# Optimization experiments

Measured on AMD Instinct MI355X. Metric: run time of the kernel, lower is better.

Reference implementation:

```python
import jax, jax.numpy as jnp
import numpy as np

B = 16384          # batch
IN = 256           # input_dim
HID = [1024, 1024, 512]
K = 8              # num_mixtures
D = 16             # latent_dim
NT = D * (D + 1) // 2  # 136 packed tril components per mixture

_rows, _cols = np.tril_indices(D)          # row-major lower-tri order, same as nested loops
_rows = jnp.asarray(_rows); _cols = jnp.asarray(_cols)
_diag_mask = _rows == _cols                # [NT] bool


def setup_inputs() -> dict:
    key = jax.random.key(0)
    ks = jax.random.split(key, 12)

    def lin(k, fi, fo):
        kw, kb = jax.random.split(k)
        s = 1.0 / np.sqrt(fi)
        W = (jax.random.uniform(kw, (fi, fo), minval=-s, maxval=s)).astype(jnp.float32)
        b = (jax.random.uniform(kb, (fo,), minval=-s, maxval=s)).astype(jnp.float32)
        return W, b

    W0, b0 = lin(ks[0], IN, HID[0])
    W1, b1 = lin(ks[1], HID[0], HID[1])
    W2, b2 = lin(ks[2], HID[1], HID[2])
    Wpi, bpi = lin(ks[3], HID[2], K)
    Wmu, bmu = lin(ks[4], HID[2], K * D)
    Wt, bt = lin(ks[5], HID[2], K * NT)
    x = jax.random.normal(ks[6], (B, IN), dtype=jnp.float32)
    return dict(x=x, W0=W0, b0=b0, W1=W1, b1=b1, W2=W2, b2=b2,
                Wpi=Wpi, bpi=bpi, Wmu=Wmu, bmu=bmu, Wt=Wt, bt=bt)


def reference(x, W0, b0, W1, b1, W2, b2, Wpi, bpi, Wmu, bmu, Wt, bt):
    # MLP trunk: Linear + ReLU chain
    h = jax.nn.relu(x @ W0 + b0)
    h = jax.nn.relu(h @ W1 + b1)
    h = jax.nn.relu(h @ W2 + b2)
    # Heads
    pi_k = jax.nn.softmax(h @ Wpi + bpi, axis=1)                 # [B, K]
    mu_k = (h @ Wmu + bmu).reshape(-1, K, D)                     # [B, K, D]
    tc = (h @ Wt + bt).reshape(-1, K, NT)                        # [B, K, NT]
    # Fused cholesky-tril assembly: exp on diagonal entries, copy off-diagonal,
    # scattered into lower triangle in row-major (i, j<=i) order.
    vals = jnp.where(_diag_mask, jnp.exp(tc), tc)                # [B, K, NT]
    tril = jnp.zeros((tc.shape[0], K, D, D), dtype=tc.dtype)
    tril = tril.at[:, :, _rows, _cols].set(vals)                 # [B, K, D, D]
    return pi_k, mu_k, tril
```

## Files before the change

### kernel.cpp

```cpp
#include <hip/hip_runtime.h>
#include <hip/hip_bf16.h>
#include <cstdint>
#include <cstddef>

typedef __attribute__((ext_vector_type(8))) _Float16 half8;
typedef __attribute__((ext_vector_type(4))) float f32x4;
typedef __attribute__((ext_vector_type(8))) unsigned short ushort8v;
typedef __attribute__((ext_vector_type(4))) unsigned short ushort4v;

__device__ __forceinline__ unsigned short f2h_bits(float x) {
  _Float16 h = (_Float16)x;
  union { _Float16 h; unsigned short u; } cv; cv.h = h; return cv.u;
}

__device__ __forceinline__ void barrier_raw() {
  asm volatile("" ::: "memory");
  __builtin_amdgcn_s_barrier();
  asm volatile("" ::: "memory");
}
template<int N> __device__ __forceinline__ void vmw() {
  static_assert(N == 0 || N == 3 || N == 4, "unsupported vmcnt");
  if constexpr (N == 0) asm volatile("s_waitcnt vmcnt(0)" ::: "memory");
  if constexpr (N == 3) asm volatile("s_waitcnt vmcnt(3)" ::: "memory");
  if constexpr (N == 4) asm volatile("s_waitcnt vmcnt(4)" ::: "memory");
}
__device__ __forceinline__ void lgkm0() {
  asm volatile("s_waitcnt lgkmcnt(0)" ::: "memory");
}


__global__ __launch_bounds__(256) void k_transpose_f16(const float* __restrict__ W,
                                                       unsigned short* __restrict__ Wt,
                                                       int Kd, int N) {
  int tid = blockIdx.x * 256 + threadIdx.x;
  int total = (Kd >> 3) * N;
  if (tid >= total) return;
  int kc = tid / N;
  int n  = tid - kc * N;
  int k0 = kc << 3;
  ushort8v o;
#pragma unroll
  for (int j = 0; j < 8; ++j) o[j] = f2h_bits(W[(size_t)(k0 + j) * N + n]);
  *(ushort8v*)(&Wt[(size_t)n * Kd + k0]) = o;
}

__global__ __launch_bounds__(256) void k_build_head(
    const float* __restrict__ Wmu, const float* __restrict__ Wt,
    const float* __restrict__ Wpi,
    const float* __restrict__ bmu, const float* __restrict__ bt,
    const float* __restrict__ bpi,
    unsigned short* __restrict__ whd, float* __restrict__ bhd)
{
  int tid = blockIdx.x * 256 + threadIdx.x;
  if (tid >= 2304 * 64) return;
  int r  = tid >> 6;
  int d0 = (tid & 63) << 3;

  const float* src = nullptr; int stride = 0;
  if (r < 128) { src = Wmu + r; stride = 128; }
  else if (r < 2176) {
    int rU = r - 128, k = rU >> 8, i = (rU >> 4) & 15, j = rU & 15;
    if (j <= i) { src = Wt + k * 136 + ((i * (i + 1)) >> 1) + j; stride = 1088; }
  } else if (r < 2184) { src = Wpi + (r - 2176); stride = 8; }

  ushort8v o;
#pragma unroll
  for (int jj = 0; jj < 8; ++jj)
    o[jj] = src ? f2h_bits(src[(size_t)(d0 + jj) * stride]) : (unsigned short)0;
  *(ushort8v*)(&whd[(size_t)r * 512 + d0]) = o;

  if (d0 == 0) {
    float b = 0.f;
    if (r < 128) b = bmu[r];
    else if (r < 2176) {
      int rU = r - 128, k = rU >> 8, i = (rU >> 4) & 15, j = rU & 15;
      if (j <= i) b = bt[k * 136 + ((i * (i + 1)) >> 1) + j];
    } else if (r < 2184) b = bpi[r - 2176];
    bhd[r] = b;
  }
}


__device__ __forceinline__ void epi_relu_h(const f32x4& a, const float* bias, int col0,
                                           unsigned short* Hout, size_t row, int N) {
  float4 b4 = *(const float4*)&bias[col0];
  ushort4v o;
  float v0 = a[0] + b4.x; o[0] = f2h_bits(v0 > 0.f ? v0 : 0.f);
  float v1 = a[1] + b4.y; o[1] = f2h_bits(v1 > 0.f ? v1 : 0.f);
  float v2 = a[2] + b4.z; o[2] = f2h_bits(v2 > 0.f ? v2 : 0.f);
  float v3 = a[3] + b4.w; o[3] = f2h_bits(v3 > 0.f ? v3 : 0.f);
  *(ushort4v*)&Hout[row * N + col0] = o;
}

__device__ __forceinline__ void epi_head(const f32x4& a, const float* bias, int col0,
                                         size_t row, float* out_pi, float* out_mu,
                                         float* out_tril) {
  if (col0 >= 2184) return;
  float4 b4 = *(const float4*)&bias[col0];
  float v[4] = { a[0] + b4.x, a[1] + b4.y, a[2] + b4.z, a[3] + b4.w };
  if (col0 < 128) {
    *(float4*)&out_mu[row * 128 + col0] = make_float4(v[0], v[1], v[2], v[3]);
  } else if (col0 < 2176) {
    const int cc0 = col0 - 128;
    const int i   = (cc0 >> 4) & 15;
    const int j0  = cc0 & 15;
#pragma unroll
    for (int r = 0; r < 4; ++r) if (j0 + r == i) v[r] = expf(v[r]);
    *(float4*)&out_tril[row * 2048 + cc0] = make_float4(v[0], v[1], v[2], v[3]);
  } else {
    float m4 = fmaxf(fmaxf(v[0], v[1]), fmaxf(v[2], v[3]));
    float mx = fmaxf(m4, __shfl_xor(m4, 16));
    float e[4], s4 = 0.f;
#pragma unroll
    for (int r = 0; r < 4; ++r) { e[r] = expf(v[r] - mx); s4 += e[r]; }
    float sm = s4 + __shfl_xor(s4, 16);
    *(float4*)&out_pi[row * 8 + (col0 - 2176)] =
        make_float4(e[0] / sm, e[1] / sm, e[2] / sm, e[3] / sm);
  }
}


__global__ __launch_bounds__(256) void k_gemm_l0(
    const float* __restrict__ X,
    const unsigned short* __restrict__ Bt,
    const float* __restrict__ bias,
    unsigned short* __restrict__ Hout)
{
  constexpr int Kd = 256, N = 1024, nNb = 8;
  __shared__ unsigned short Ald[2][128 * 32];
  __shared__ unsigned short Bld[2][128 * 32];

  const int tid  = threadIdx.x;
  const int lane = tid & 63;
  const int wv   = tid >> 6;
  const int wr   = wv >> 1;
  const int wc   = wv & 1;
  const int l15  = lane & 15;
  const int lk   = lane >> 4;

  const int cpx = gridDim.x >> 3;
  const int bid = blockIdx.x;
  const int swz = (bid & 7) * cpx + (bid >> 3);
  const int bm  = (swz / nNb) << 7;
  const int bn  = (swz % nNb) << 7;

  f32x4 acc[4][4] = {};

  const float*          aBase = X  + (size_t)bm * Kd;
  const unsigned short* bBase = Bt + (size_t)bn * Kd;

  const int xo = ((lk ^ ((l15 >> 1) & 3)) << 3);

  const int c0   = (wv << 6) + lane;
  const int c1   = c0 + 256;
  const int row0 = c0 >> 2, row1 = c1 >> 2;
  const int sc0  = (((c0 & 3) ^ ((c0 >> 3) & 3)) << 3);
  const int sc1  = (((c1 & 3) ^ ((c1 >> 3) & 3)) << 3);

  auto issueB = [&](int bb, int kt) {
    const int k0 = kt << 5;
#pragma unroll
    for (int i = 0; i < 2; ++i) {
      const int cbase = (wv << 6) + (i << 8);
      const int c_    = cbase + lane;
      const int row   = c_ >> 2;
      const int sc    = (((c_ & 3) ^ ((c_ >> 3) & 3)) << 3);
      __builtin_amdgcn_global_load_lds(
          (const __attribute__((address_space(1))) void*)(bBase + (size_t)row * Kd + k0 + sc),
          (__attribute__((address_space(3))) void*)(&Bld[bb][cbase << 3]),
          16, 0, 0);
    }
  };

  float4 p0, p1, p2, p3;
  auto loadA = [&](int kt) {
    const int k0 = kt << 5;
    const float* s0 = aBase + (size_t)row0 * Kd + k0 + sc0;
    const float* s1 = aBase + (size_t)row1 * Kd + k0 + sc1;
    p0 = *(const float4*)(s0);
    p1 = *(const float4*)(s0 + 4);
    p2 = *(const float4*)(s1);
    p3 = *(const float4*)(s1 + 4);
  };
  auto writeA = [&](int bb) {
    half8 h0, h1;
    h0[0]=(_Float16)p0.x; h0[1]=(_Float16)p0.y; h0[2]=(_Float16)p0.z; h0[3]=(_Float16)p0.w;
    h0[4]=(_Float16)p1.x; h0[5]=(_Float16)p1.y; h0[6]=(_Float16)p1.z; h0[7]=(_Float16)p1.w;
    h1[0]=(_Float16)p2.x; h1[1]=(_Float16)p2.y; h1[2]=(_Float16)p2.z; h1[3]=(_Float16)p2.w;
    h1[4]=(_Float16)p3.x; h1[5]=(_Float16)p3.y; h1[6]=(_Float16)p3.z; h1[7]=(_Float16)p3.w;
    *(half8*)&Ald[bb][c0 << 3] = h0;
    *(half8*)&Ald[bb][c1 << 3] = h1;
  };

  const int nk = Kd >> 5;
  loadA(0); issueB(0, 0); writeA(0);
  __syncthreads();

  int cur = 0;
  for (int kt = 0; kt < nk; ++kt) {
    const bool pre = (kt + 1 < nk);
    if (pre) { loadA(kt + 1); issueB(cur ^ 1, kt + 1); }

    half8 af[4], bfr[4];
#pragma unroll
    for (int m = 0; m < 4; ++m)
      af[m]  = *(const half8*)&Ald[cur][((wr << 6) + (m << 4) + l15) * 32 + xo];
#pragma unroll
    for (int n = 0; n < 4; ++n)
      bfr[n] = *(const half8*)&Bld[cur][((wc << 6) + (n << 4) + l15) * 32 + xo];

    __builtin_amdgcn_s_setprio(1);
#pragma unroll
    for (int m = 0; m < 4; ++m)
#pragma unroll
      for (int n = 0; n < 4; ++n)
        acc[m][n] = __builtin_amdgcn_mfma_f32_16x16x32_f16(bfr[n], af[m], acc[m][n], 0, 0, 0);
    __builtin_amdgcn_s_setprio(0);

    if (pre) writeA(cur ^ 1);
    __syncthreads();
    cur ^= 1;
  }

#pragma unroll
  for (int m = 0; m < 4; ++m) {
    const size_t row = bm + (wr << 6) + (m << 4) + l15;
#pragma unroll
    for (int n = 0; n < 4; ++n) {
      const int col0 = bn + (wc << 6) + (n << 4) + (lk << 2);
      epi_relu_h(acc[m][n], bias, col0, Hout, row, N);
    }
  }
}


template<int EPI>
__global__ __launch_bounds__(256) void k_gemm3b(
    const unsigned short* __restrict__ A,
    const unsigned short* __restrict__ Bt,
    int Kd, int N, int nNb,
    const float* __restrict__ bias,
    unsigned short* __restrict__ Hout,
    float* __restrict__ out_pi,
    float* __restrict__ out_mu,
    float* __restrict__ out_tril)
{
  __shared__ unsigned short Ald[3][128 * 32];
  __shared__ unsigned short Bld[3][128 * 32];

  const int tid  = threadIdx.x;
  const int lane = tid & 63;
  const int wv   = tid >> 6;
  const int wr   = wv >> 1;
  const int wc   = wv & 1;
  const int l15  = lane & 15;
  const int lk   = lane >> 4;

  const int cpx = gridDim.x >> 3;
  const int bid = blockIdx.x;
  const int swz = (bid & 7) * cpx + (bid >> 3);
  const int bm  = (swz / nNb) << 7;
  const int bn  = (swz % nNb) << 7;

  f32x4 acc[4][4] = {};

  const unsigned short* aBase = A  + (size_t)bm * Kd;
  const unsigned short* bBase = Bt + (size_t)bn * Kd;

  const int xo = ((lk ^ ((l15 >> 1) & 3)) << 3);

  auto stage = [&](int bb, int kt) {
    const int k0 = kt << 5;
#pragma unroll
    for (int i = 0; i < 2; ++i) {
      const int cbase = (wv << 6) + (i << 8);
      const int c_    = cbase + lane;
      const int row   = c_ >> 2;
      const int sc    = (((c_ & 3) ^ ((c_ >> 3) & 3)) << 3);
      __builtin_amdgcn_global_load_lds(
          (const __attribute__((address_space(1))) void*)(aBase + (size_t)row * Kd + k0 + sc),
          (__attribute__((address_space(3))) void*)(&Ald[bb][cbase << 3]),
          16, 0, 0);
      __builtin_amdgcn_global_load_lds(
          (const __attribute__((address_space(1))) void*)(bBase + (size_t)row * Kd + k0 + sc),
          (__attribute__((address_space(3))) void*)(&Bld[bb][cbase << 3]),
          16, 0, 0);
    }
  };

  const int nk = Kd >> 5;
  stage(0, 0);
  stage(1, 1);
  vmw<4>();
  barrier_raw();

  int i0 = 0, i1 = 1, i2 = 2;
  for (int kt = 0; kt < nk; ++kt) {
    if (kt + 2 < nk) stage(i2, kt + 2);

    half8 af[4], bfr[4];
#pragma unroll
    for (int m = 0; m < 4; ++m)
      af[m]  = *(const half8*)&Ald[i0][((wr << 6) + (m << 4) + l15) * 32 + xo];
#pragma unroll
    for (int n = 0; n < 4; ++n)
      bfr[n] = *(const half8*)&Bld[i0][((wc << 6) + (n << 4) + l15) * 32 + xo];

    __builtin_amdgcn_s_setprio(1);
#pragma unroll
    for (int m = 0; m < 4; ++m)
#pragma unroll
      for (int n = 0; n < 4; ++n)
        acc[m][n] = __builtin_amdgcn_mfma_f32_16x16x32_f16(bfr[n], af[m], acc[m][n], 0, 0, 0);
    __builtin_amdgcn_s_setprio(0);

    if (kt + 1 < nk) {
      if (kt + 2 < nk) vmw<4>();
      else             vmw<0>();
      barrier_raw();
    }
    const int t = i0; i0 = i1; i1 = i2; i2 = t;
  }

#pragma unroll
  for (int m = 0; m < 4; ++m) {
    const size_t row = bm + (wr << 6) + (m << 4) + l15;
#pragma unroll
    for (int n = 0; n < 4; ++n) {
      const int col0 = bn + (wc << 6) + (n << 4) + (lk << 2);
      if (EPI == 0) epi_relu_h(acc[m][n], bias, col0, Hout, row, N);
      else          epi_head(acc[m][n], bias, col0, row, out_pi, out_mu, out_tril);
    }
  }
}


template<int NH, int M_rep>
__device__ __forceinline__ void mfma_phase(const half8* af, const half8* bf,
                                           f32x4 (*acc)[4]) {
  __builtin_amdgcn_s_setprio(1);
#pragma unroll
  for (int m = 0; m < M_rep; ++m) {
    acc[m][NH * 2 + 0] = __builtin_amdgcn_mfma_f32_16x16x32_f16(bf[0], af[m], acc[m][NH * 2 + 0], 0, 0, 0);
    acc[m][NH * 2 + 1] = __builtin_amdgcn_mfma_f32_16x16x32_f16(bf[1], af[m], acc[m][NH * 2 + 1], 0, 0, 0);
  }
  __builtin_amdgcn_s_setprio(0);
}

template<int BM, int BN>
__global__ __launch_bounds__(512) void k_gemm8p(
    const unsigned short* __restrict__ A,
    const unsigned short* __restrict__ Bt,
    int Kd, int N, int nNb,
    const float* __restrict__ bias,
    unsigned short* __restrict__ Hout)
{
  constexpr int M_rep = BM / 32;
  constexpr int A_LD  = BM / 128;
  constexpr int B_LD  = BN / 128;
  constexpr int WN    = A_LD + B_LD;

  __shared__ unsigned short Ald[2][2][BM * 32];
  __shared__ unsigned short Bld[2][2][BN * 32];

  const int tid  = threadIdx.x;
  const int lane = tid & 63;
  const int wid  = tid >> 6;
  const int wm   = wid >> 2;
  const int wn   = wid & 3;
  const int l15  = lane & 15;
  const int lk   = lane >> 4;

  const int cpx = gridDim.x >> 3;
  const int bid = blockIdx.x;
  const int swz = (bid & 7) * cpx + (bid >> 3);
  const int bm  = (swz / nNb) * BM;
  const int bn  = (swz % nNb) * BN;

  const unsigned short* aBase = A  + (size_t)bm * Kd;
  const unsigned short* bBase = Bt + (size_t)bn * Kd;

  f32x4 acc[M_rep][4] = {};

  const int xo   = ((lk ^ ((l15 >> 1) & 3)) << 3);
  const int rowA = wm * (BM / 2) + l15;
  const int colB = wn * 64 + l15;

  auto stageA = [&](int bb, int h, int k0) {
#pragma unroll
    for (int i = 0; i < A_LD; ++i) {
      const int cbase = (wid << 6) + (i << 9);
      const int c_    = cbase + lane;
      const int row   = c_ >> 2;
      const int sc    = (((c_ & 3) ^ ((c_ >> 3) & 3)) << 3);
      __builtin_amdgcn_global_load_lds(
          (const __attribute__((address_space(1))) void*)(aBase + (size_t)row * Kd + k0 + h * 32 + sc),
          (__attribute__((address_space(3))) void*)(&Ald[bb][h][(size_t)cbase << 3]),
          16, 0, 0);
    }
  };
  auto stageB = [&](int bb, int h, int k0) {
#pragma unroll
    for (int i = 0; i < B_LD; ++i) {
      const int cbase = (wid << 6) + (i << 9);
      const int c_    = cbase + lane;
      const int row   = c_ >> 2;
      const int sc    = (((c_ & 3) ^ ((c_ >> 3) & 3)) << 3);
      __builtin_amdgcn_global_load_lds(
          (const __attribute__((address_space(1))) void*)(bBase + (size_t)row * Kd + k0 + h * 32 + sc),
          (__attribute__((address_space(3))) void*)(&Bld[bb][h][(size_t)cbase << 3]),
          16, 0, 0);
    }
  };

#define RD_A(kk)                                                                 \
  {                                                                              \
    _Pragma("unroll")                                                            \
    for (int m = 0; m < M_rep; ++m)                                              \
      af[m] = *(const half8*)&Ald[cur][kk][(size_t)(rowA + m * 16) * 32 + xo];   \
  }
#define RD_B(kk, nh)                                                             \
  {                                                                              \
    _Pragma("unroll")                                                            \
    for (int n2 = 0; n2 < 2; ++n2)                                               \
      bf[n2] = *(const half8*)&Bld[cur][kk][(size_t)(colB + ((nh) * 2 + n2) * 16) * 32 + xo]; \
  }

  const int nk = Kd >> 6;
  stageA(0, 0, 0); stageB(0, 0, 0); stageA(0, 1, 0); stageB(0, 1, 0);
  vmw<WN>();
  barrier_raw();

  int cur = 0;
  for (int kt = 0; kt < nk; ++kt) {
    const bool pre = (kt + 1 < nk);
    const int  k0n = (kt + 1) << 6;
    half8 af[M_rep], bf[2];

    RD_A(0); RD_B(0, 0);
    if (pre) stageA(cur ^ 1, 0, k0n);
    barrier_raw(); lgkm0();
    mfma_phase<0, M_rep>(af, bf, acc);
    barrier_raw();

    RD_B(0, 1);
    if (pre) stageB(cur ^ 1, 0, k0n);
    barrier_raw(); lgkm0();
    mfma_phase<1, M_rep>(af, bf, acc);
    if (pre) vmw<WN>(); else vmw<0>();
    barrier_raw();

    RD_A(1); RD_B(1, 0);
    if (pre) stageA(cur ^ 1, 1, k0n);
    barrier_raw(); lgkm0();
    mfma_phase<0, M_rep>(af, bf, acc);
    barrier_raw();

    RD_B(1, 1);
    if (pre) stageB(cur ^ 1, 1, k0n);
    barrier_raw(); lgkm0();
    mfma_phase<1, M_rep>(af, bf, acc);
    if (pre) vmw<WN>();
    barrier_raw();

    cur ^= 1;
  }
#undef RD_A
#undef RD_B

#pragma unroll
  for (int m = 0; m < M_rep; ++m) {
    const size_t row = bm + wm * (BM / 2) + (m << 4) + l15;
#pragma unroll
    for (int n = 0; n < 4; ++n) {
      const int col0 = bn + wn * 64 + (n << 4) + (lk << 2);
      epi_relu_h(acc[m][n], bias, col0, Hout, row, N);
    }
  }
}


extern "C" void kernel_launch(void* const* d_in, const int* in_sizes, int n_in,
                              void* d_out, int out_size, void* d_ws, size_t ws_size,
                              hipStream_t stream)
{
  const float* x   = (const float*)d_in[0];
  const float* W0  = (const float*)d_in[1];
  const float* b0  = (const float*)d_in[2];
  const float* W1  = (const float*)d_in[3];
  const float* b1  = (const float*)d_in[4];
  const float* W2  = (const float*)d_in[5];
  const float* b2  = (const float*)d_in[6];
  const float* Wpi = (const float*)d_in[7];
  const float* bpi = (const float*)d_in[8];
  const float* Wmu = (const float*)d_in[9];
  const float* bmu = (const float*)d_in[10];
  const float* Wt  = (const float*)d_in[11];
  const float* bt  = (const float*)d_in[12];

  char* ws = (char*)d_ws;
  unsigned short* h0  = (unsigned short*)(ws + 8388608);
  unsigned short* h1  = (unsigned short*)(ws + 41943040);
  unsigned short* h2  = (unsigned short*)(ws + 8388608);
  unsigned short* w0b = (unsigned short*)(ws + 75497472);
  unsigned short* w1b = (unsigned short*)(ws + 76021760);
  unsigned short* w2b = (unsigned short*)(ws + 78118912);
  unsigned short* whd = (unsigned short*)(ws + 79167488);
  float*          bhd = (float*)         (ws + 81526784);

  float* out_pi   = (float*)d_out;
  float* out_mu   = (float*)d_out + 131072;
  float* out_tril = (float*)d_out + 2228224;

  k_transpose_f16<<<128, 256, 0, stream>>>(W0, w0b, 256, 1024);
  k_transpose_f16<<<512, 256, 0, stream>>>(W1, w1b, 1024, 1024);
  k_transpose_f16<<<256, 256, 0, stream>>>(W2, w2b, 1024, 512);
  k_build_head<<<576, 256, 0, stream>>>(Wmu, Wt, Wpi, bmu, bt, bpi, whd, bhd);

  k_gemm_l0<<<1024, 256, 0, stream>>>(x, w0b, b0, h0);
  k_gemm8p<256, 256><<<256, 512, 0, stream>>>(h0, w1b, 1024, 1024, 4, b1, h1);
  k_gemm8p<128, 256><<<256, 512, 0, stream>>>(h1, w2b, 1024, 512, 2, b2, h2);
  k_gemm3b<1><<<2304, 256, 0, stream>>>(h2, whd, 512, 2304, 18, bhd, nullptr,
                                        out_pi, out_mu, out_tril);
}
```

Before: 186.6 us.

## Load head GEMM A operand directly into registers, staging only B through LDS

Replaces the generic head GEMM with a specialized kernel where each wave loads its A fragments straight from global memory into registers using inline global_load_dwordx4. Only B is staged through a triple-buffered LDS ring, and the K loop is fully unrolled with explicit vmcnt waits and sched barriers. This halves LDS traffic and LDS footprint per block, allowing more occupancy via launch_bounds(256,4). It risks uncoalesced A reads, since each lane fetches 16 bytes per row, and it depends on hand-tuned waitcnt counts that must match the inline-asm load ordering.

```diff
diff --git a/kernel.cpp b/kernel.cpp
--- a/kernel.cpp
+++ b/kernel.cpp
@@ -19,13 +19,20 @@
   asm volatile("" ::: "memory");
 }
 template<int N> __device__ __forceinline__ void vmw() {
-  static_assert(N == 0 || N == 3 || N == 4, "unsupported vmcnt");
+  static_assert(N == 0 || N == 3 || N == 4 || N == 6, "unsupported vmcnt");
   if constexpr (N == 0) asm volatile("s_waitcnt vmcnt(0)" ::: "memory");
   if constexpr (N == 3) asm volatile("s_waitcnt vmcnt(3)" ::: "memory");
   if constexpr (N == 4) asm volatile("s_waitcnt vmcnt(4)" ::: "memory");
+  if constexpr (N == 6) asm volatile("s_waitcnt vmcnt(6)" ::: "memory");
 }
 __device__ __forceinline__ void lgkm0() {
   asm volatile("s_waitcnt lgkmcnt(0)" ::: "memory");
+}
+
+__device__ __forceinline__ half8 gload16(const unsigned short* p) {
+  half8 r;
+  asm volatile("global_load_dwordx4 %0, %1, off" : "=v"(r) : "v"(p));
+  return r;
 }
 
 
@@ -120,6 +127,129 @@
 }
 
 
+__global__ __launch_bounds__(256, 4) void k_head_areg(
+    const unsigned short* __restrict__ A,
+    const unsigned short* __restrict__ Bt,
+    const float* __restrict__ bias,
+    float* __restrict__ out_pi,
+    float* __restrict__ out_mu,
+    float* __restrict__ out_tril)
+{
+  constexpr int Kd = 512, nNb = 18;
+  __shared__ unsigned short Bld[3][128 * 32];
+
+  const int tid  = threadIdx.x;
+  const int lane = tid & 63;
+  const int wv   = tid >> 6;
+  const int wr   = wv >> 1;
+  const int wc   = wv & 1;
+  const int l15  = lane & 15;
+  const int lk   = lane >> 4;
+
+  const int cpx = gridDim.x >> 3;
+  const int bid = blockIdx.x;
+  const int swz = (bid & 7) * cpx + (bid >> 3);
+  const int bm  = (swz / nNb) << 7;
+  const int bn  = (swz % nNb) << 7;
+
+  f32x4 acc[4][4] = {};
+
+  const unsigned short* a0p = A + (size_t)(bm + (wr << 6) + 0  + l15) * Kd + (lk << 3);
+  const unsigned short* a1p = a0p + (size_t)16 * Kd;
+  const unsigned short* a2p = a0p + (size_t)32 * Kd;
+  const unsigned short* a3p = a0p + (size_t)48 * Kd;
+
+  const unsigned short* bBase = Bt + (size_t)bn * Kd;
+  const int xo   = ((lk ^ ((l15 >> 1) & 3)) << 3);
+  const int colB = (wc << 6) + l15;
+
+  auto stageB = [&](int bb, int kt) {
+    const int k0 = kt << 5;
+#pragma unroll
+    for (int i = 0; i < 2; ++i) {
+      const int c_  = (wv << 6) + (i << 8) + lane;
+      const int row = c_ >> 2;
+      const int sc  = (((c_ & 3) ^ ((c_ >> 3) & 3)) << 3);
+      __builtin_amdgcn_global_load_lds(
+          (const __attribute__((address_space(1))) void*)(bBase + (size_t)row * Kd + k0 + sc),
+          (__attribute__((address_space(3))) void*)(&Bld[bb][((wv << 6) + (i << 8)) << 3]),
+          16, 0, 0);
+    }
+  };
+
+  half8 aE0, aE1, aE2, aE3, aO0, aO1, aO2, aO3;
+
+#define AISSUE(S, t) do {                 \
+    a##S##0 = gload16(a0p + (t) * 32);    \
+    a##S##1 = gload16(a1p + (t) * 32);    \
+    a##S##2 = gload16(a2p + (t) * 32);    \
+    a##S##3 = gload16(a3p + (t) * 32);    \
+  } while (0)
+
+#define HCOMP(S, b) do {                                                                   \
+    half8 bf0 = *(const half8*)&Bld[b][(size_t)(colB + 0)  * 32 + xo];                     \
+    half8 bf1 = *(const half8*)&Bld[b][(size_t)(colB + 16) * 32 + xo];                     \
+    half8 bf2 = *(const half8*)&Bld[b][(size_t)(colB + 32) * 32 + xo];                     \
+    half8 bf3 = *(const half8*)&Bld[b][(size_t)(colB + 48) * 32 + xo];                     \
+    __builtin_amdgcn_s_setprio(1);                                                        \
+    acc[0][0] = __builtin_amdgcn_mfma_f32_16x16x32_f16(bf0, a##S##0, acc[0][0], 0, 0, 0); \
+    acc[0][1] = __builtin_amdgcn_mfma_f32_16x16x32_f16(bf1, a##S##0, acc[0][1], 0, 0, 0); \
+    acc[0][2] = __builtin_amdgcn_mfma_f32_16x16x32_f16(bf2, a##S##0, acc[0][2], 0, 0, 0); \
+    acc[0][3] = __builtin_amdgcn_mfma_f32_16x16x32_f16(bf3, a##S##0, acc[0][3], 0, 0, 0); \
+    acc[1][0] = __builtin_amdgcn_mfma_f32_16x16x32_f16(bf0, a##S##1, acc[1][0], 0, 0, 0); \
+    acc[1][1] = __builtin_amdgcn_mfma_f32_16x16x32_f16(bf1, a##S##1, acc[1][1], 0, 0, 0); \
+    acc[1][2] = __builtin_amdgcn_mfma_f32_16x16x32_f16(bf2, a##S##1, acc[1][2], 0, 0, 0); \
+    acc[1][3] = __builtin_amdgcn_mfma_f32_16x16x32_f16(bf3, a##S##1, acc[1][3], 0, 0, 0); \
+    acc[2][0] = __builtin_amdgcn_mfma_f32_16x16x32_f16(bf0, a##S##2, acc[2][0], 0, 0, 0); \
+    acc[2][1] = __builtin_amdgcn_mfma_f32_16x16x32_f16(bf1, a##S##2, acc[2][1], 0, 0, 0); \
+    acc[2][2] = __builtin_amdgcn_mfma_f32_16x16x32_f16(bf2, a##S##2, acc[2][2], 0, 0, 0); \
+    acc[2][3] = __builtin_amdgcn_mfma_f32_16x16x32_f16(bf3, a##S##2, acc[2][3], 0, 0, 0); \
+    acc[3][0] = __builtin_amdgcn_mfma_f32_16x16x32_f16(bf0, a##S##3, acc[3][0], 0, 0, 0); \
+    acc[3][1] = __builtin_amdgcn_mfma_f32_16x16x32_f16(bf1, a##S##3, acc[3][1], 0, 0, 0); \
+    acc[3][2] = __builtin_amdgcn_mfma_f32_16x16x32_f16(bf2, a##S##3, acc[3][2], 0, 0, 0); \
+    acc[3][3] = __builtin_amdgcn_mfma_f32_16x16x32_f16(bf3, a##S##3, acc[3][3], 0, 0, 0); \
+    __builtin_amdgcn_s_setprio(0);                                                        \
+    __builtin_amdgcn_sched_barrier(0);                                                    \
+  } while (0)
+
+#define SB __builtin_amdgcn_sched_barrier(0)
+  stageB(0, 0); stageB(1, 1);
+  AISSUE(E, 0);
+  vmw<4>(); SB;
+  barrier_raw();
+
+  stageB(2, 2);  AISSUE(O, 1);  vmw<6>(); SB; HCOMP(E, 0); barrier_raw();
+  stageB(0, 3);  AISSUE(E, 2);  vmw<6>(); SB; HCOMP(O, 1); barrier_raw();
+  stageB(1, 4);  AISSUE(O, 3);  vmw<6>(); SB; HCOMP(E, 2); barrier_raw();
+  stageB(2, 5);  AISSUE(E, 4);  vmw<6>(); SB; HCOMP(O, 0); barrier_raw();
+  stageB(0, 6);  AISSUE(O, 5);  vmw<6>(); SB; HCOMP(E, 1); barrier_raw();
+  stageB(1, 7);  AISSUE(E, 6);  vmw<6>(); SB; HCOMP(O, 2); barrier_raw();
+  stageB(2, 8);  AISSUE(O, 7);  vmw<6>(); SB; HCOMP(E, 0); barrier_raw();
+  stageB(0, 9);  AISSUE(E, 8);  vmw<6>(); SB; HCOMP(O, 1); barrier_raw();
+  stageB(1, 10); AISSUE(O, 9);  vmw<6>(); SB; HCOMP(E, 2); barrier_raw();
+  stageB(2, 11); AISSUE(E, 10); vmw<6>(); SB; HCOMP(O, 0); barrier_raw();
+  stageB(0, 12); AISSUE(O, 11); vmw<6>(); SB; HCOMP(E, 1); barrier_raw();
+  stageB(1, 13); AISSUE(E, 12); vmw<6>(); SB; HCOMP(O, 2); barrier_raw();
+  stageB(2, 14); AISSUE(O, 13); vmw<6>(); SB; HCOMP(E, 0); barrier_raw();
+  stageB(0, 15); AISSUE(E, 14); vmw<6>(); SB; HCOMP(O, 1); barrier_raw();
+  AISSUE(O, 15); vmw<4>(); SB; HCOMP(E, 2); barrier_raw();
+  vmw<0>(); SB; HCOMP(O, 0);
+#undef AISSUE
+#undef HCOMP
+#undef SB
+
+#pragma unroll
+  for (int m = 0; m < 4; ++m) {
+    const size_t row = bm + (wr << 6) + (m << 4) + l15;
+#pragma unroll
+    for (int n = 0; n < 4; ++n) {
+      const int col0 = bn + (wc << 6) + (n << 4) + (lk << 2);
+      epi_head(acc[m][n], bias, col0, row, out_pi, out_mu, out_tril);
+    }
+  }
+}
+
+
 __global__ __launch_bounds__(256) void k_gemm_l0(
     const float* __restrict__ X,
     const unsigned short* __restrict__ Bt,
@@ -127,8 +257,8 @@
     unsigned short* __restrict__ Hout)
 {
   constexpr int Kd = 256, N = 1024, nNb = 8;
-  __shared__ unsigned short Ald[2][128 * 32];
-  __shared__ unsigned short Bld[2][128 * 32];
+  __shared__ unsigned short Alds[2][128 * 32];
+  __shared__ unsigned short Blds[2][128 * 32];
 
   const int tid  = threadIdx.x;
   const int lane = tid & 63;
@@ -167,7 +297,7 @@
       const int sc    = (((c_ & 3) ^ ((c_ >> 3) & 3)) << 3);
       __builtin_amdgcn_global_load_lds(
           (const __attribute__((address_space(1))) void*)(bBase + (size_t)row * Kd + k0 + sc),
-          (__attribute__((address_space(3))) void*)(&Bld[bb][cbase << 3]),
+          (__attribute__((address_space(3))) void*)(&Blds[bb][cbase << 3]),
           16, 0, 0);
     }
   };
@@ -188,8 +318,8 @@
     h0[4]=(_Float16)p1.x; h0[5]=(_Float16)p1.y; h0[6]=(_Float16)p1.z; h0[7]=(_Float16)p1.w;
     h1[0]=(_Float16)p2.x; h1[1]=(_Float16)p2.y; h1[2]=(_Float16)p2.z; h1[3]=(_Float16)p2.w;
     h1[4]=(_Float16)p3.x; h1[5]=(_Float16)p3.y; h1[6]=(_Float16)p3.z; h1[7]=(_Float16)p3.w;
-    *(half8*)&Ald[bb][c0 << 3] = h0;
-    *(half8*)&Ald[bb][c1 << 3] = h1;
+    *(half8*)&Alds[bb][c0 << 3] = h0;
+    *(half8*)&Alds[bb][c1 << 3] = h1;
   };
 
   const int nk = Kd >> 5;
@@ -204,10 +334,10 @@
     half8 af[4], bfr[4];
 #pragma unroll
     for (int m = 0; m < 4; ++m)
-      af[m]  = *(const half8*)&Ald[cur][((wr << 6) + (m << 4) + l15) * 32 + xo];
+      af[m]  = *(const half8*)&Alds[cur][((wr << 6) + (m << 4) + l15) * 32 + xo];
 #pragma unroll
     for (int n = 0; n < 4; ++n)
-      bfr[n] = *(const half8*)&Bld[cur][((wc << 6) + (n << 4) + l15) * 32 + xo];
+      bfr[n] = *(const half8*)&Blds[cur][((wc << 6) + (n << 4) + l15) * 32 + xo];
 
     __builtin_amdgcn_s_setprio(1);
 #pragma unroll
@@ -229,107 +359,6 @@
     for (int n = 0; n < 4; ++n) {
       const int col0 = bn + (wc << 6) + (n << 4) + (lk << 2);
       epi_relu_h(acc[m][n], bias, col0, Hout, row, N);
-    }
-  }
-}
-
-
-template<int EPI>
-__global__ __launch_bounds__(256) void k_gemm3b(
-    const unsigned short* __restrict__ A,
-    const unsigned short* __restrict__ Bt,
-    int Kd, int N, int nNb,
-    const float* __restrict__ bias,
-    unsigned short* __restrict__ Hout,
-    float* __restrict__ out_pi,
-    float* __restrict__ out_mu,
-    float* __restrict__ out_tril)
-{
-  __shared__ unsigned short Ald[3][128 * 32];
-  __shared__ unsigned short Bld[3][128 * 32];
-
-  const int tid  = threadIdx.x;
-  const int lane = tid & 63;
-  const int wv   = tid >> 6;
-  const int wr   = wv >> 1;
-  const int wc   = wv & 1;
-  const int l15  = lane & 15;
-  const int lk   = lane >> 4;
-
-  const int cpx = gridDim.x >> 3;
-  const int bid = blockIdx.x;
-  const int swz = (bid & 7) * cpx + (bid >> 3);
-  const int bm  = (swz / nNb) << 7;
-  const int bn  = (swz % nNb) << 7;
-
-  f32x4 acc[4][4] = {};
-
-  const unsigned short* aBase = A  + (size_t)bm * Kd;
-  const unsigned short* bBase = Bt + (size_t)bn * Kd;
-
-  const int xo = ((lk ^ ((l15 >> 1) & 3)) << 3);
-
-  auto stage = [&](int bb, int kt) {
-    const int k0 = kt << 5;
-#pragma unroll
-    for (int i = 0; i < 2; ++i) {
-      const int cbase = (wv << 6) + (i << 8);
-      const int c_    = cbase + lane;
-      const int row   = c_ >> 2;
-      const int sc    = (((c_ & 3) ^ ((c_ >> 3) & 3)) << 3);
-      __builtin_amdgcn_global_load_lds(
-          (const __attribute__((address_space(1))) void*)(aBase + (size_t)row * Kd + k0 + sc),
-          (__attribute__((address_space(3))) void*)(&Ald[bb][cbase << 3]),
-          16, 0, 0);
-      __builtin_amdgcn_global_load_lds(
-          (const __attribute__((address_space(1))) void*)(bBase + (size_t)row * Kd + k0 + sc),
-          (__attribute__((address_space(3))) void*)(&Bld[bb][cbase << 3]),
-          16, 0, 0);
-    }
-  };
-
-  const int nk = Kd >> 5;
-  stage(0, 0);
-  stage(1, 1);
-  vmw<4>();
-  barrier_raw();
-
-  int i0 = 0, i1 = 1, i2 = 2;
-  for (int kt = 0; kt < nk; ++kt) {
-    if (kt + 2 < nk) stage(i2, kt + 2);
-
-    half8 af[4], bfr[4];
-#pragma unroll
-    for (int m = 0; m < 4; ++m)
-      af[m]  = *(const half8*)&Ald[i0][((wr << 6) + (m << 4) + l15) * 32 + xo];
-#pragma unroll
-    for (int n = 0; n < 4; ++n)
-      bfr[n] = *(const half8*)&Bld[i0][((wc << 6) + (n << 4) + l15) * 32 + xo];
-
-    __builtin_amdgcn_s_setprio(1);
-#pragma unroll
-    for (int m = 0; m < 4; ++m)
-#pragma unroll
-      for (int n = 0; n < 4; ++n)
-        acc[m][n] = __builtin_amdgcn_mfma_f32_16x16x32_f16(bfr[n], af[m], acc[m][n], 0, 0, 0);
-    __builtin_amdgcn_s_setprio(0);
-
-    if (kt + 1 < nk) {
-      if (kt + 2 < nk) vmw<4>();
-      else             vmw<0>();
-      barrier_raw();
-    }
-    const int t = i0; i0 = i1; i1 = i2; i2 = t;
-  }
-
-#pragma unroll
-  for (int m = 0; m < 4; ++m) {
-    const size_t row = bm + (wr << 6) + (m << 4) + l15;
-#pragma unroll
-    for (int n = 0; n < 4; ++n) {
-      const int col0 = bn + (wc << 6) + (n << 4) + (lk << 2);
-      if (EPI == 0) epi_relu_h(acc[m][n], bias, col0, Hout, row, N);
-      else          epi_head(acc[m][n], bias, col0, row, out_pi, out_mu, out_tril);
     }
   }
 }
@@ -428,7 +457,7 @@
 
   const int nk = Kd >> 6;
   stageA(0, 0, 0); stageB(0, 0, 0); stageA(0, 1, 0); stageB(0, 1, 0);
-  vmw<WN>();
+  { if constexpr (WN == 3) vmw<3>(); else vmw<4>(); }
   barrier_raw();
 
   int cur = 0;
@@ -447,7 +476,7 @@
     if (pre) stageB(cur ^ 1, 0, k0n);
     barrier_raw(); lgkm0();
     mfma_phase<1, M_rep>(af, bf, acc);
-    if (pre) vmw<WN>(); else vmw<0>();
+    if (pre) { if constexpr (WN == 3) vmw<3>(); else vmw<4>(); } else vmw<0>();
     barrier_raw();
 
     RD_A(1); RD_B(1, 0);
@@ -460,7 +489,7 @@
     if (pre) stageB(cur ^ 1, 1, k0n);
     barrier_raw(); lgkm0();
     mfma_phase<1, M_rep>(af, bf, acc);
-    if (pre) vmw<WN>();
+    if (pre) { if constexpr (WN == 3) vmw<3>(); else vmw<4>(); }
     barrier_raw();
 
     cur ^= 1;
@@ -520,6 +549,5 @@
   k_gemm_l0<<<1024, 256, 0, stream>>>(x, w0b, b0, h0);
   k_gemm8p<256, 256><<<256, 512, 0, stream>>>(h0, w1b, 1024, 1024, 4, b1, h1);
   k_gemm8p<128, 256><<<256, 512, 0, stream>>>(h1, w2b, 1024, 512, 2, b2, h2);
-  k_gemm3b<1><<<2304, 256, 0, stream>>>(h2, whd, 512, 2304, 18, bhd, nullptr,
-                                        out_pi, out_mu, out_tril);
-}
+  k_head_areg<<<2304, 256, 0, stream>>>(h2, whd, bhd, out_pi, out_mu, out_tril);
+}
```

Result: slower. 221.1 us (+18.5%).
